# Performance work log

Hardware: AMD Instinct MI355X
Metric: run time of the kernel (lower is better)

Reference implementation:

```python
import jax, jax.numpy as jnp
import numpy as np

B, T, E = 2, 2048, 1024
NEXP, TOPK, INTER = 8, 2, 1408


def setup_inputs() -> dict:
    key = jax.random.key(0)
    ks = jax.random.split(key, 5)
    s = 0.02
    return {
        "x": jax.random.normal(ks[0], (B, T, E), dtype=jnp.float32),
        "gate_w": jax.random.normal(ks[1], (NEXP, E), dtype=jnp.float32) * s,
        "wg": jax.random.normal(ks[2], (NEXP, INTER, E), dtype=jnp.float32) * s,
        "wu": jax.random.normal(ks[3], (NEXP, INTER, E), dtype=jnp.float32) * s,
        "wd": jax.random.normal(ks[4], (NEXP, E, INTER), dtype=jnp.float32) * s,
    }


def reference(x, gate_w, wg, wu, wd):
    # Router: scores [B,T,NEXP], topk softmax over selected experts only
    scores = jnp.einsum("btd,ed->bte", x, gate_w)
    topk_scores, topk_idx = jax.lax.top_k(scores, TOPK)  # [B,T,K]
    topk_probs = jax.nn.softmax(topk_scores, axis=-1)
    # Scatter back to dense gating probs [B,T,NEXP] (topk indices are unique)
    onehot = jax.nn.one_hot(topk_idx, NEXP, dtype=x.dtype)  # [B,T,K,NEXP]
    gating = jnp.sum(onehot * topk_probs[..., None], axis=-2)  # [B,T,NEXP]
    # Dense compute-all-experts (faithful to the original module)
    g = jnp.einsum("btd,eid->btei", x, wg)  # [B,T,NEXP,INTER]
    u = jnp.einsum("btd,eid->btei", x, wu)
    h = jax.nn.silu(g) * u
    expert_out = jnp.einsum("btei,edi->bted", h, wd)  # [B,T,NEXP,E]
    y = jnp.sum(gating[..., None] * expert_out, axis=-2)  # [B,T,E]
    return y
```

## Files before the change

kernel.cpp:

```cpp
#include <hip/hip_runtime.h>
#include <hip/hip_bf16.h>
#include <stdint.h>

typedef __hip_bfloat16 bf16;
typedef __attribute__((ext_vector_type(8))) short short8;
typedef __attribute__((ext_vector_type(4))) float f32x4;

#define NTOK  4096
#define EDIM  1024
#define NEXPT 8
#define INTERD 1408
#define MAXP  4096
#define WELEM (NEXPT * INTERD * EDIM)

#define GL16(g, l) __builtin_amdgcn_global_load_lds( \
    (const __attribute__((address_space(1))) unsigned int*)(g), \
    (__attribute__((address_space(3))) unsigned int*)(l), 16, 0, 0)

#define WAIT_VM(n)   asm volatile("s_waitcnt vmcnt(" #n ")" ::: "memory")
#define BAR()        __builtin_amdgcn_s_barrier()
#define PRIO(n)      __builtin_amdgcn_s_setprio(n)

__global__ __launch_bounds__(256) void prep_kernel(const float* __restrict__ wg, bf16* __restrict__ wgb,
                                                   const float* __restrict__ wu, bf16* __restrict__ wub,
                                                   const float* __restrict__ wd, bf16* __restrict__ wdb,
                                                   const float* __restrict__ x,
                                                   const float* __restrict__ gw,
                                                   bf16* __restrict__ xb,
                                                   int* __restrict__ sel,
                                                   float* __restrict__ tprob) {
    int b = blockIdx.x;
    if (b < 3072) {
        const float* src; bf16* dst;
        if (b < 1024)      { src = wg; dst = wgb; }
        else if (b < 2048) { src = wu; dst = wub; b -= 1024; }
        else               { src = wd; dst = wdb; b -= 2048; }
        int i = (b * 256 + threadIdx.x) * 4;
        int stride = 1024 * 256 * 4;
        for (; i < WELEM; i += stride) {
            float4 v = *(const float4*)(src + i);
            ushort4 o; bf16 t;
            t = __float2bfloat16(v.x); o.x = *(unsigned short*)&t;
            t = __float2bfloat16(v.y); o.y = *(unsigned short*)&t;
            t = __float2bfloat16(v.z); o.z = *(unsigned short*)&t;
            t = __float2bfloat16(v.w); o.w = *(unsigned short*)&t;
            *(ushort4*)(dst + i) = o;
        }
        return;
    }
    int t = (b - 3072) * 4 + (threadIdx.x >> 6);
    int lane = threadIdx.x & 63;
    const float* xr = x + (size_t)t * EDIM;
    float xv[16];
#pragma unroll
    for (int j = 0; j < 4; j++) {
        float4 v = *(const float4*)(xr + lane * 16 + j * 4);
        xv[4 * j] = v.x; xv[4 * j + 1] = v.y; xv[4 * j + 2] = v.z; xv[4 * j + 3] = v.w;
    }
    bf16* xbr = xb + (size_t)t * EDIM;
#pragma unroll
    for (int j = 0; j < 4; j++) {
        ushort4 o; bf16 c;
        c = __float2bfloat16(xv[4 * j]);     o.x = *(unsigned short*)&c;
        c = __float2bfloat16(xv[4 * j + 1]); o.y = *(unsigned short*)&c;
        c = __float2bfloat16(xv[4 * j + 2]); o.z = *(unsigned short*)&c;
        c = __float2bfloat16(xv[4 * j + 3]); o.w = *(unsigned short*)&c;
        *(ushort4*)(xbr + lane * 16 + j * 4) = o;
    }
    double acc[NEXPT];
#pragma unroll
    for (int e = 0; e < NEXPT; e++) acc[e] = 0.0;
#pragma unroll
    for (int e = 0; e < NEXPT; e++) {
        const float* gr = gw + e * EDIM + lane * 16;
#pragma unroll
        for (int j = 0; j < 16; j++) acc[e] += (double)xv[j] * (double)gr[j];
    }
#pragma unroll
    for (int off = 32; off >= 1; off >>= 1) {
#pragma unroll
        for (int e = 0; e < NEXPT; e++) acc[e] += __shfl_xor(acc[e], off, 64);
    }
    if (lane == 0) {
        int e0 = 0; double s0 = acc[0];
        for (int e = 1; e < NEXPT; e++) if (acc[e] > s0) { s0 = acc[e]; e0 = e; }
        int e1 = -1; double s1 = -1e300;
        for (int e = 0; e < NEXPT; e++) if (e != e0 && acc[e] > s1) { s1 = acc[e]; e1 = e; }
        float z = __expf((float)(s1 - s0));
        float p0 = 1.f / (1.f + z);
        sel[t] = e0 | (e1 << 8);
        tprob[2 * t] = p0;
        tprob[2 * t + 1] = 1.f - p0;
    }
}

__global__ __launch_bounds__(512) void bucket_kernel(const int* __restrict__ sel,
                                                     const float* __restrict__ tprob,
                                                     int* __restrict__ counts,
                                                     int* __restrict__ offsets,
                                                     int* __restrict__ ptok,
                                                     float* __restrict__ pprob,
                                                     int* __restrict__ inv,
                                                     int* __restrict__ wq1,
                                                     int* __restrict__ wq2) {
    __shared__ int scnt[NEXPT];
    int w = threadIdx.x >> 6;
    int lane = threadIdx.x & 63;
    unsigned long long ltmask = (lane == 63) ? ~0ull >> 1 : (1ull << lane) - 1;
    int base = 0;
    for (int t0 = 0; t0 < NTOK; t0 += 64) {
        int t = t0 + lane;
        int s = sel[t];
        int e0 = s & 0xff, e1 = (s >> 8) & 0xff;
        unsigned long long m0 = __ballot(e0 == w);
        if (e0 == w) {
            int pos = base + __popcll(m0 & ltmask);
            ptok[w * MAXP + pos] = t;
            pprob[w * MAXP + pos] = tprob[2 * t];
            inv[2 * t] = (w << 16) | pos;
        }
        base += __popcll(m0);
        unsigned long long m1 = __ballot(e1 == w);
        if (e1 == w) {
            int pos = base + __popcll(m1 & ltmask);
            ptok[w * MAXP + pos] = t;
            pprob[w * MAXP + pos] = tprob[2 * t + 1];
            inv[2 * t + 1] = (w << 16) | pos;
        }
        base += __popcll(m1);
    }
    if (lane == 0) scnt[w] = base;
    __syncthreads();
    if (threadIdx.x < NEXPT) {
        int off = 0;
        for (int e = 0; e < (int)threadIdx.x; e++) off += scnt[e];
        counts[threadIdx.x] = scnt[threadIdx.x];
        offsets[threadIdx.x] = off;
        wq1[threadIdx.x * 32] = 0;
        wq2[threadIdx.x * 32] = 0;
    }
}

__global__ __launch_bounds__(512, 4) void gemm1_kernel(const bf16* __restrict__ xb,
                                                       const bf16* __restrict__ wgb,
                                                       const bf16* __restrict__ wub,
                                                       bf16* __restrict__ hout,
                                                       const int* __restrict__ counts,
                                                       const int* __restrict__ offsets,
                                                       const int* __restrict__ ptok,
                                                       const float* __restrict__ pprob,
                                                       int* __restrict__ wq1) {
    int eown = blockIdx.x & 7;

    __shared__ __align__(16) bf16 smem[3 * 12288];
    __shared__ int s_wi;

    int tid  = threadIdx.x;
    int lane = tid & 63;
    int wid  = tid >> 6;
    int wm   = wid >> 2;
    int wn   = wid & 3;

    int srow = tid >> 2;
    int qs   = (((tid & 3) ^ ((srow >> 1) & 3)) * 8);
    int l15  = lane & 15;
    int l4   = lane >> 4;

    int offA[4], offG[2];
#pragma unroll
    for (int m = 0; m < 4; m++) {
        int r = wm * 64 + m * 16 + l15;
        offA[m] = r * 32 + ((l4 ^ ((r >> 1) & 3)) * 8);
    }
#pragma unroll
    for (int n = 0; n < 2; n++) {
        int r = wn * 32 + n * 16 + l15;
        offG[n] = r * 32 + ((l4 ^ ((r >> 1) & 3)) * 8);
    }

    for (int ei = 0; ei < NEXPT; ++ei) {
        int e = (eown + ei) & 7;
        int cnt = counts[e];
        int mtiles = (cnt + 127) >> 7;
        int tiles = mtiles * (INTERD / 128);
        int hbase = offsets[e];

        for (;;) {
            if (tid == 0) s_wi = atomicAdd(&wq1[e * 32], 1);
            __syncthreads();
            int wi = s_wi;
            __syncthreads();
            if (wi >= tiles) break;
            int mt = wi % mtiles;
            int nt = wi / mtiles;
            int m0 = mt * 128;
            int n0 = nt * 128;

            WAIT_VM(0);
            const bf16* gA = xb + (size_t)ptok[e * MAXP + min(m0 + srow, cnt - 1)] * EDIM + qs;
            const bf16* gG = wgb + ((size_t)e * INTERD + n0 + srow) * EDIM + qs;
            const bf16* gU = wub + ((size_t)e * INTERD + n0 + srow) * EDIM + qs;

            f32x4 accg[4][2], accu[4][2];
#pragma unroll
            for (int m = 0; m < 4; m++)
#pragma unroll
                for (int n = 0; n < 2; n++) {
                    accg[m][n] = (f32x4){0.f, 0.f, 0.f, 0.f};
                    accu[m][n] = (f32x4){0.f, 0.f, 0.f, 0.f};
                }

#define SB1(t) (smem + ((t) % 3) * 12288)
#define G1_STAGE(t) do { bf16* sb_ = SB1(t); int ko_ = (t) * 32; \
            GL16(gA + ko_, sb_ + wid * 512); \
            GL16(gG + ko_, sb_ + 4096 + wid * 512); \
            GL16(gU + ko_, sb_ + 8192 + wid * 512); } while (0)

            G1_STAGE(0); G1_STAGE(1);

            for (int t = 0; t < 32; ++t) {
                if (t < 30)       { G1_STAGE(t + 2); WAIT_VM(6); }
                else if (t == 30) { WAIT_VM(3); }
                else              { WAIT_VM(0); }
                BAR();
                const bf16* sb = SB1(t);
                short8 a_[4], gf[2], uf[2];
#pragma unroll
                for (int m = 0; m < 4; m++) a_[m] = *(const short8*)&sb[offA[m]];
#pragma unroll
                for (int n = 0; n < 2; n++) {
                    gf[n] = *(const short8*)&sb[4096 + offG[n]];
                    uf[n] = *(const short8*)&sb[8192 + offG[n]];
                }
                PRIO(1);
#pragma unroll
                for (int m = 0; m < 4; m++)
#pragma unroll
                    for (int n = 0; n < 2; n++) {
                        accg[m][n] = __builtin_amdgcn_mfma_f32_16x16x32_bf16(a_[m], gf[n], accg[m][n], 0, 0, 0);
                        accu[m][n] = __builtin_amdgcn_mfma_f32_16x16x32_bf16(a_[m], uf[n], accu[m][n], 0, 0, 0);
                    }
                PRIO(0);
                BAR();
            }
#undef SB1
#undef G1_STAGE

#pragma unroll
            for (int m = 0; m < 4; m++)
#pragma unroll
                for (int n = 0; n < 2; n++)
#pragma unroll
                    for (int r = 0; r < 4; r++) {
                        int pos = m0 + wm * 64 + m * 16 + l4 * 4 + r;
                        if (pos < cnt) {
                            int col = n0 + wn * 32 + n * 16 + l15;
                            float p = pprob[e * MAXP + pos];
                            float gv = accg[m][n][r];
                            float uv = accu[m][n][r];
                            float hv = (gv / (1.f + __expf(-gv))) * uv * p;
                            hout[(size_t)(hbase + pos) * INTERD + col] = __float2bfloat16(hv);
                        }
                    }
        }
    }
}

__global__ __launch_bounds__(512, 4) void gemm2_kernel(const bf16* __restrict__ h,
                                                       const bf16* __restrict__ wdb,
                                                       bf16* __restrict__ out2,
                                                       const int* __restrict__ counts,
                                                       const int* __restrict__ offsets,
                                                       int* __restrict__ wq2) {
    int eown = blockIdx.x & 7;

    __shared__ __align__(16) bf16 smem[3 * 8192];
    __shared__ int s_wi;

    int tid  = threadIdx.x;
    int lane = tid & 63;
    int wid  = tid >> 6;
    int wm   = wid >> 2;
    int wn   = wid & 3;

    int srow = tid >> 2;
    int qs   = (((tid & 3) ^ ((srow >> 1) & 3)) * 8);
    int l15  = lane & 15;
    int l4   = lane >> 4;

    int offA[4], offB[2];
#pragma unroll
    for (int m = 0; m < 4; m++) {
        int r = wm * 64 + m * 16 + l15;
        offA[m] = r * 32 + ((l4 ^ ((r >> 1) & 3)) * 8);
    }
#pragma unroll
    for (int n = 0; n < 2; n++) {
        int r = wn * 32 + n * 16 + l15;
        offB[n] = 4096 + r * 32 + ((l4 ^ ((r >> 1) & 3)) * 8);
    }

    for (int ei = 0; ei < NEXPT; ++ei) {
        int e = (eown + ei) & 7;
        int cnt = counts[e];
        int mtiles = (cnt + 127) >> 7;
        int tiles = mtiles * (EDIM / 128);
        int hbase = offsets[e];

        for (;;) {
            if (tid == 0) s_wi = atomicAdd(&wq2[e * 32], 1);
            __syncthreads();
            int wi = s_wi;
            __syncthreads();
            if (wi >= tiles) break;
            int mt = wi % mtiles;
            int nt = wi / mtiles;
            int m0 = mt * 128;
            int n0 = nt * 128;

            WAIT_VM(0);
            const bf16* gA = h + (size_t)(hbase + min(m0 + srow, cnt - 1)) * INTERD + qs;
            const bf16* gB = wdb + ((size_t)e * EDIM + n0 + srow) * INTERD + qs;

            f32x4 acc[4][2];
#pragma unroll
            for (int m = 0; m < 4; m++)
#pragma unroll
                for (int n = 0; n < 2; n++) acc[m][n] = (f32x4){0.f, 0.f, 0.f, 0.f};

#define SB2(t) (smem + ((t) % 3) * 8192)
#define G2_STAGE(t) do { bf16* sb_ = SB2(t); int ko_ = (t) * 32; \
            GL16(gA + ko_, sb_ + wid * 512); \
            GL16(gB + ko_, sb_ + 4096 + wid * 512); } while (0)

            G2_STAGE(0); G2_STAGE(1);

            for (int t = 0; t < 44; ++t) {
                if (t < 42)       { G2_STAGE(t + 2); WAIT_VM(4); }
                else if (t == 42) { WAIT_VM(2); }
                else              { WAIT_VM(0); }
                BAR();
                const bf16* sb = SB2(t);
                short8 a_[4], b_[2];
#pragma unroll
                for (int m = 0; m < 4; m++) a_[m] = *(const short8*)&sb[offA[m]];
#pragma unroll
                for (int n = 0; n < 2; n++) b_[n] = *(const short8*)&sb[offB[n]];
                PRIO(1);
#pragma unroll
                for (int m = 0; m < 4; m++)
#pragma unroll
                    for (int n = 0; n < 2; n++)
                        acc[m][n] = __builtin_amdgcn_mfma_f32_16x16x32_bf16(a_[m], b_[n], acc[m][n], 0, 0, 0);
                PRIO(0);
                BAR();
            }
#undef SB2
#undef G2_STAGE

#pragma unroll
            for (int m = 0; m < 4; m++)
#pragma unroll
                for (int n = 0; n < 2; n++)
#pragma unroll
                    for (int r = 0; r < 4; r++) {
                        int pos = m0 + wm * 64 + m * 16 + l4 * 4 + r;
                        if (pos < cnt) {
                            int col = n0 + wn * 32 + n * 16 + l15;
                            out2[(size_t)(hbase + pos) * EDIM + col] = __float2bfloat16(acc[m][n][r]);
                        }
                    }
        }
    }
}

__global__ __launch_bounds__(256) void combine_kernel(const bf16* __restrict__ out2,
                                                      const int* __restrict__ inv,
                                                      const int* __restrict__ offsets,
                                                      float* __restrict__ y) {
    int idx = blockIdx.x * 256 + threadIdx.x;
    int t = idx >> 7;
    int c = (idx & 127) * 8;
    int a = inv[2 * t], b = inv[2 * t + 1];
    const short8 va = *(const short8*)(out2 + (size_t)(offsets[a >> 16] + (a & 0xFFFF)) * EDIM + c);
    const short8 vb = *(const short8*)(out2 + (size_t)(offsets[b >> 16] + (b & 0xFFFF)) * EDIM + c);
    float o[8];
#pragma unroll
    for (int j = 0; j < 8; j++) {
        unsigned ua = ((unsigned)(unsigned short)va[j]) << 16;
        unsigned ub = ((unsigned)(unsigned short)vb[j]) << 16;
        o[j] = *(float*)&ua + *(float*)&ub;
    }
    float* yp = y + (size_t)t * EDIM + c;
    *(float4*)yp       = (float4){o[0], o[1], o[2], o[3]};
    *(float4*)(yp + 4) = (float4){o[4], o[5], o[6], o[7]};
}

extern "C" void kernel_launch(void* const* d_in, const int* in_sizes, int n_in,
                              void* d_out, int out_size, void* d_ws, size_t ws_size,
                              hipStream_t stream) {
    const float* x      = (const float*)d_in[0];
    const float* gate_w = (const float*)d_in[1];
    const float* wg     = (const float*)d_in[2];
    const float* wu     = (const float*)d_in[3];
    const float* wd     = (const float*)d_in[4];
    float* y = (float*)d_out;

    char* ws = (char*)d_ws;
    constexpr size_t SZ_XB = (size_t)NTOK * EDIM * 2;
    constexpr size_t SZ_W  = (size_t)WELEM * 2;
    constexpr size_t SZ_H  = (size_t)NTOK * 2 * INTERD * 2;
    bf16* xb  = (bf16*)ws;
    bf16* wgb = (bf16*)(ws + SZ_XB);
    bf16* wub = (bf16*)(ws + SZ_XB + SZ_W);
    bf16* wdb = (bf16*)(ws + SZ_XB + 2 * SZ_W);
    bf16* h   = (bf16*)(ws + SZ_XB + 3 * SZ_W);
    char* meta = ws + SZ_XB + 3 * SZ_W + SZ_H;
    int*   counts  = (int*)meta;
    int*   offsets = (int*)(meta + 256);
    int*   ptok    = (int*)(meta + 512);
    float* pprob   = (float*)(meta + 512 + (size_t)NEXPT * MAXP * 4);
    int*   inv     = (int*)(meta + 512 + (size_t)NEXPT * MAXP * 8);
    char*  meta2   = meta + 512 + (size_t)NEXPT * MAXP * 8 + (size_t)NTOK * 2 * 4;
    int*   wq1     = (int*)meta2;
    int*   wq2     = (int*)(meta2 + 1024);
    int*   sel     = (int*)(meta2 + 2048);
    float* tprob   = (float*)(meta2 + 2048 + (size_t)NTOK * 4);
    bf16* out2 = (bf16*)(ws + SZ_XB);

    prep_kernel<<<3072 + NTOK / 4, 256, 0, stream>>>(wg, wgb, wu, wub, wd, wdb,
                                                     x, gate_w, xb, sel, tprob);
    bucket_kernel<<<1, 512, 0, stream>>>(sel, tprob, counts, offsets, ptok, pprob, inv,
                                         wq1, wq2);

    gemm1_kernel<<<512, 512, 0, stream>>>(
        xb, wgb, wub, h, counts, offsets, ptok, pprob, wq1);
    gemm2_kernel<<<512, 512, 0, stream>>>(
        h, wdb, out2, counts, offsets, wq2);
    combine_kernel<<<NTOK * EDIM / 8 / 256, 256, 0, stream>>>(out2, inv, offsets, y);
}
```

Measured before the change: 230.1 us.

## Fuse combine into gemm2 via atomic scatter-add and enlarge per-wave tile

Removes the separate combine kernel and the bf16 out2 intermediate. gemm2 now scatter-adds fp32 results directly into y using ptok and atomicAdd, and y is zeroed with a memset beforehand. gemm2 is also changed to 256 threads with each wave computing a 64x64 sub-tile, doubling MFMA work per LDS load. This trades the intermediate write/read and one launch for 8M float atomics, which may contend, and makes the summation order nondeterministic.

```diff
diff --git a/kernel.cpp b/kernel.cpp
--- a/kernel.cpp
+++ b/kernel.cpp
@@ -100,7 +100,6 @@
                                                      int* __restrict__ offsets,
                                                      int* __restrict__ ptok,
                                                      float* __restrict__ pprob,
-                                                     int* __restrict__ inv,
                                                      int* __restrict__ wq1,
                                                      int* __restrict__ wq2) {
     __shared__ int scnt[NEXPT];
@@ -117,7 +116,6 @@
             int pos = base + __popcll(m0 & ltmask);
             ptok[w * MAXP + pos] = t;
             pprob[w * MAXP + pos] = tprob[2 * t];
-            inv[2 * t] = (w << 16) | pos;
         }
         base += __popcll(m0);
         unsigned long long m1 = __ballot(e1 == w);
@@ -125,7 +123,6 @@
             int pos = base + __popcll(m1 & ltmask);
             ptok[w * MAXP + pos] = t;
             pprob[w * MAXP + pos] = tprob[2 * t + 1];
-            inv[2 * t + 1] = (w << 16) | pos;
         }
         base += __popcll(m1);
     }
@@ -266,11 +263,12 @@
     }
 }
 
-__global__ __launch_bounds__(512, 4) void gemm2_kernel(const bf16* __restrict__ h,
+__global__ __launch_bounds__(256, 2) void gemm2_kernel(const bf16* __restrict__ h,
                                                        const bf16* __restrict__ wdb,
-                                                       bf16* __restrict__ out2,
+                                                       float* __restrict__ y,
                                                        const int* __restrict__ counts,
                                                        const int* __restrict__ offsets,
+                                                       const int* __restrict__ ptok,
                                                        int* __restrict__ wq2) {
     int eown = blockIdx.x & 7;
 
@@ -280,23 +278,23 @@
     int tid  = threadIdx.x;
     int lane = tid & 63;
     int wid  = tid >> 6;
-    int wm   = wid >> 2;
-    int wn   = wid & 3;
+    int wm   = wid >> 1;
+    int wn   = wid & 1;
 
     int srow = tid >> 2;
     int qs   = (((tid & 3) ^ ((srow >> 1) & 3)) * 8);
     int l15  = lane & 15;
     int l4   = lane >> 4;
 
-    int offA[4], offB[2];
+    int offA[4], offB[4];
 #pragma unroll
     for (int m = 0; m < 4; m++) {
         int r = wm * 64 + m * 16 + l15;
         offA[m] = r * 32 + ((l4 ^ ((r >> 1) & 3)) * 8);
     }
 #pragma unroll
-    for (int n = 0; n < 2; n++) {
-        int r = wn * 32 + n * 16 + l15;
+    for (int n = 0; n < 4; n++) {
+        int r = wn * 64 + n * 16 + l15;
         offB[n] = 4096 + r * 32 + ((l4 ^ ((r >> 1) & 3)) * 8);
     }
 
@@ -319,38 +317,42 @@
             int n0 = nt * 128;
 
             WAIT_VM(0);
-            const bf16* gA = h + (size_t)(hbase + min(m0 + srow, cnt - 1)) * INTERD + qs;
-            const bf16* gB = wdb + ((size_t)e * EDIM + n0 + srow) * INTERD + qs;
-
-            f32x4 acc[4][2];
+            const bf16* gA0 = h + (size_t)(hbase + min(m0 + srow,      cnt - 1)) * INTERD + qs;
+            const bf16* gA1 = h + (size_t)(hbase + min(m0 + 64 + srow, cnt - 1)) * INTERD + qs;
+            const bf16* gB0 = wdb + ((size_t)e * EDIM + n0 + srow) * INTERD + qs;
+            const bf16* gB1 = wdb + ((size_t)e * EDIM + n0 + 64 + srow) * INTERD + qs;
+
+            f32x4 acc[4][4];
 #pragma unroll
             for (int m = 0; m < 4; m++)
 #pragma unroll
-                for (int n = 0; n < 2; n++) acc[m][n] = (f32x4){0.f, 0.f, 0.f, 0.f};
+                for (int n = 0; n < 4; n++) acc[m][n] = (f32x4){0.f, 0.f, 0.f, 0.f};
 
 #define SB2(t) (smem + ((t) % 3) * 8192)
 #define G2_STAGE(t) do { bf16* sb_ = SB2(t); int ko_ = (t) * 32; \
-            GL16(gA + ko_, sb_ + wid * 512); \
-            GL16(gB + ko_, sb_ + 4096 + wid * 512); } while (0)
+            GL16(gA0 + ko_, sb_ + wid * 512); \
+            GL16(gA1 + ko_, sb_ + 2048 + wid * 512); \
+            GL16(gB0 + ko_, sb_ + 4096 + wid * 512); \
+            GL16(gB1 + ko_, sb_ + 6144 + wid * 512); } while (0)
 
             G2_STAGE(0); G2_STAGE(1);
 
             for (int t = 0; t < 44; ++t) {
-                if (t < 42)       { G2_STAGE(t + 2); WAIT_VM(4); }
-                else if (t == 42) { WAIT_VM(2); }
+                if (t < 42)       { G2_STAGE(t + 2); WAIT_VM(8); }
+                else if (t == 42) { WAIT_VM(4); }
                 else              { WAIT_VM(0); }
                 BAR();
                 const bf16* sb = SB2(t);
-                short8 a_[4], b_[2];
+                short8 a_[4], b_[4];
 #pragma unroll
                 for (int m = 0; m < 4; m++) a_[m] = *(const short8*)&sb[offA[m]];
 #pragma unroll
-                for (int n = 0; n < 2; n++) b_[n] = *(const short8*)&sb[offB[n]];
+                for (int n = 0; n < 4; n++) b_[n] = *(const short8*)&sb[offB[n]];
                 PRIO(1);
 #pragma unroll
                 for (int m = 0; m < 4; m++)
 #pragma unroll
-                    for (int n = 0; n < 2; n++)
+                    for (int n = 0; n < 4; n++)
                         acc[m][n] = __builtin_amdgcn_mfma_f32_16x16x32_bf16(a_[m], b_[n], acc[m][n], 0, 0, 0);
                 PRIO(0);
                 BAR();
@@ -359,41 +361,23 @@
 #undef G2_STAGE
 
 #pragma unroll
-            for (int m = 0; m < 4; m++)
-#pragma unroll
-                for (int n = 0; n < 2; n++)
-#pragma unroll
-                    for (int r = 0; r < 4; r++) {
-                        int pos = m0 + wm * 64 + m * 16 + l4 * 4 + r;
-                        if (pos < cnt) {
-                            int col = n0 + wn * 32 + n * 16 + l15;
-                            out2[(size_t)(hbase + pos) * EDIM + col] = __float2bfloat16(acc[m][n][r]);
-                        }
-                    }
+            for (int m = 0; m < 4; m++) {
+                int pos = m0 + wm * 64 + m * 16 + l4 * 4;
+                int tok[4];
+#pragma unroll
+                for (int r = 0; r < 4; r++)
+                    tok[r] = (pos + r < cnt) ? ptok[e * MAXP + pos + r] : -1;
+#pragma unroll
+                for (int n = 0; n < 4; n++) {
+                    int col = n0 + wn * 64 + n * 16 + l15;
+#pragma unroll
+                    for (int r = 0; r < 4; r++)
+                        if (tok[r] >= 0)
+                            atomicAdd(&y[(size_t)tok[r] * EDIM + col], acc[m][n][r]);
+                }
+            }
         }
     }
-}
-
-__global__ __launch_bounds__(256) void combine_kernel(const bf16* __restrict__ out2,
-                                                      const int* __restrict__ inv,
-                                                      const int* __restrict__ offsets,
-                                                      float* __restrict__ y) {
-    int idx = blockIdx.x * 256 + threadIdx.x;
-    int t = idx >> 7;
-    int c = (idx & 127) * 8;
-    int a = inv[2 * t], b = inv[2 * t + 1];
-    const short8 va = *(const short8*)(out2 + (size_t)(offsets[a >> 16] + (a & 0xFFFF)) * EDIM + c);
-    const short8 vb = *(const short8*)(out2 + (size_t)(offsets[b >> 16] + (b & 0xFFFF)) * EDIM + c);
-    float o[8];
-#pragma unroll
-    for (int j = 0; j < 8; j++) {
-        unsigned ua = ((unsigned)(unsigned short)va[j]) << 16;
-        unsigned ub = ((unsigned)(unsigned short)vb[j]) << 16;
-        o[j] = *(float*)&ua + *(float*)&ub;
-    }
-    float* yp = y + (size_t)t * EDIM + c;
-    *(float4*)yp       = (float4){o[0], o[1], o[2], o[3]};
-    *(float4*)(yp + 4) = (float4){o[4], o[5], o[6], o[7]};
 }
 
 extern "C" void kernel_launch(void* const* d_in, const int* in_sizes, int n_in,
@@ -420,22 +404,21 @@
     int*   offsets = (int*)(meta + 256);
     int*   ptok    = (int*)(meta + 512);
     float* pprob   = (float*)(meta + 512 + (size_t)NEXPT * MAXP * 4);
-    int*   inv     = (int*)(meta + 512 + (size_t)NEXPT * MAXP * 8);
-    char*  meta2   = meta + 512 + (size_t)NEXPT * MAXP * 8 + (size_t)NTOK * 2 * 4;
+    char*  meta2   = meta + 512 + (size_t)NEXPT * MAXP * 8;
     int*   wq1     = (int*)meta2;
     int*   wq2     = (int*)(meta2 + 1024);
     int*   sel     = (int*)(meta2 + 2048);
     float* tprob   = (float*)(meta2 + 2048 + (size_t)NTOK * 4);
-    bf16* out2 = (bf16*)(ws + SZ_XB);
+
+    hipMemsetAsync(d_out, 0, (size_t)out_size * 4, stream);
 
     prep_kernel<<<3072 + NTOK / 4, 256, 0, stream>>>(wg, wgb, wu, wub, wd, wdb,
                                                      x, gate_w, xb, sel, tprob);
-    bucket_kernel<<<1, 512, 0, stream>>>(sel, tprob, counts, offsets, ptok, pprob, inv,
+    bucket_kernel<<<1, 512, 0, stream>>>(sel, tprob, counts, offsets, ptok, pprob,
                                          wq1, wq2);
 
     gemm1_kernel<<<512, 512, 0, stream>>>(
         xb, wgb, wub, h, counts, offsets, ptok, pprob, wq1);
-    gemm2_kernel<<<512, 512, 0, stream>>>(
-        h, wdb, out2, counts, offsets, wq2);
-    combine_kernel<<<NTOK * EDIM / 8 / 256, 256, 0, stream>>>(out2, inv, offsets, y);
+    gemm2_kernel<<<512, 256, 0, stream>>>(
+        h, wdb, y, counts, offsets, ptok, wq2);
 }
```

Result: slower. 249.8 us (+8.6%).

## Widen gemm2 tiles to 128x256 and replace atomic work queue with static grid

Applied to the files above, without the earlier changes.

The down-projection GEMM now uses 128x256 output tiles, so each wave computes a 64x64 sub-tile and each A tile loaded into shared memory feeds twice as many MFMAs. The atomic-counter work queue is replaced by a fixed grid of 256 blocks indexed by expert, M-slot and N-tile, and each block strides over M in steps of 1024. This removes the per-tile atomic and the barriers around it and increases reuse of the A tile. In exchange it uses more accumulator registers and LDS, and load balance across experts becomes static, so a skewed routing distribution can leave some blocks with more work than others.

```diff
diff --git a/kernel.cpp b/kernel.cpp
--- a/kernel.cpp
+++ b/kernel.cpp
@@ -270,12 +270,16 @@
                                                        const bf16* __restrict__ wdb,
                                                        bf16* __restrict__ out2,
                                                        const int* __restrict__ counts,
-                                                       const int* __restrict__ offsets,
-                                                       int* __restrict__ wq2) {
-    int eown = blockIdx.x & 7;
-
-    __shared__ __align__(16) bf16 smem[3 * 8192];
-    __shared__ int s_wi;
+                                                       const int* __restrict__ offsets) {
+    int bx = blockIdx.x;
+    int e  = bx & 7;
+    int mt = (bx >> 3) & 7;
+    int nt = bx >> 6;
+    int cnt = counts[e];
+    int n0 = nt * 256;
+    int hbase = offsets[e];
+
+    __shared__ __align__(16) bf16 smem[3 * 12288];
 
     int tid  = threadIdx.x;
     int lane = tid & 63;
@@ -288,89 +292,74 @@
     int l15  = lane & 15;
     int l4   = lane >> 4;
 
-    int offA[4], offB[2];
+    int offA[4], offB[4];
 #pragma unroll
     for (int m = 0; m < 4; m++) {
         int r = wm * 64 + m * 16 + l15;
         offA[m] = r * 32 + ((l4 ^ ((r >> 1) & 3)) * 8);
     }
 #pragma unroll
-    for (int n = 0; n < 2; n++) {
-        int r = wn * 32 + n * 16 + l15;
+    for (int n = 0; n < 4; n++) {
+        int r = wn * 64 + n * 16 + l15;
         offB[n] = 4096 + r * 32 + ((l4 ^ ((r >> 1) & 3)) * 8);
     }
 
-    for (int ei = 0; ei < NEXPT; ++ei) {
-        int e = (eown + ei) & 7;
-        int cnt = counts[e];
-        int mtiles = (cnt + 127) >> 7;
-        int tiles = mtiles * (EDIM / 128);
-        int hbase = offsets[e];
-
-        for (;;) {
-            if (tid == 0) s_wi = atomicAdd(&wq2[e * 32], 1);
-            __syncthreads();
-            int wi = s_wi;
-            __syncthreads();
-            if (wi >= tiles) break;
-            int mt = wi % mtiles;
-            int nt = wi / mtiles;
-            int m0 = mt * 128;
-            int n0 = nt * 128;
-
-            WAIT_VM(0);
-            const bf16* gA = h + (size_t)(hbase + min(m0 + srow, cnt - 1)) * INTERD + qs;
-            const bf16* gB = wdb + ((size_t)e * EDIM + n0 + srow) * INTERD + qs;
-
-            f32x4 acc[4][2];
+    const bf16* gB0 = wdb + ((size_t)e * EDIM + n0 + srow) * INTERD + qs;
+    const bf16* gB1 = wdb + ((size_t)e * EDIM + n0 + 128 + srow) * INTERD + qs;
+
+    for (int m0 = mt * 128; m0 < cnt; m0 += 1024) {
+        WAIT_VM(0);
+        const bf16* gA = h + (size_t)(hbase + min(m0 + srow, cnt - 1)) * INTERD + qs;
+
+        f32x4 acc[4][4];
+#pragma unroll
+        for (int m = 0; m < 4; m++)
+#pragma unroll
+            for (int n = 0; n < 4; n++) acc[m][n] = (f32x4){0.f, 0.f, 0.f, 0.f};
+
+#define SB2(t) (smem + ((t) % 3) * 12288)
+#define G2_STAGE(t) do { bf16* sb_ = SB2(t); int ko_ = (t) * 32; \
+        GL16(gA + ko_,  sb_ + wid * 512); \
+        GL16(gB0 + ko_, sb_ + 4096 + wid * 512); \
+        GL16(gB1 + ko_, sb_ + 8192 + wid * 512); } while (0)
+
+        G2_STAGE(0); G2_STAGE(1);
+
+        for (int t = 0; t < 44; ++t) {
+            if (t < 42)       { G2_STAGE(t + 2); WAIT_VM(6); }
+            else if (t == 42) { WAIT_VM(3); }
+            else              { WAIT_VM(0); }
+            BAR();
+            const bf16* sb = SB2(t);
+            short8 a_[4], b_[4];
+#pragma unroll
+            for (int m = 0; m < 4; m++) a_[m] = *(const short8*)&sb[offA[m]];
+#pragma unroll
+            for (int n = 0; n < 4; n++) b_[n] = *(const short8*)&sb[offB[n]];
+            PRIO(1);
 #pragma unroll
             for (int m = 0; m < 4; m++)
 #pragma unroll
-                for (int n = 0; n < 2; n++) acc[m][n] = (f32x4){0.f, 0.f, 0.f, 0.f};
-
-#define SB2(t) (smem + ((t) % 3) * 8192)
-#define G2_STAGE(t) do { bf16* sb_ = SB2(t); int ko_ = (t) * 32; \
-            GL16(gA + ko_, sb_ + wid * 512); \
-            GL16(gB + ko_, sb_ + 4096 + wid * 512); } while (0)
-
-            G2_STAGE(0); G2_STAGE(1);
-
-            for (int t = 0; t < 44; ++t) {
-                if (t < 42)       { G2_STAGE(t + 2); WAIT_VM(4); }
-                else if (t == 42) { WAIT_VM(2); }
-                else              { WAIT_VM(0); }
-                BAR();
-                const bf16* sb = SB2(t);
-                short8 a_[4], b_[2];
-#pragma unroll
-                for (int m = 0; m < 4; m++) a_[m] = *(const short8*)&sb[offA[m]];
-#pragma unroll
-                for (int n = 0; n < 2; n++) b_[n] = *(const short8*)&sb[offB[n]];
-                PRIO(1);
-#pragma unroll
-                for (int m = 0; m < 4; m++)
-#pragma unroll
-                    for (int n = 0; n < 2; n++)
-                        acc[m][n] = __builtin_amdgcn_mfma_f32_16x16x32_bf16(a_[m], b_[n], acc[m][n], 0, 0, 0);
-                PRIO(0);
-                BAR();
-            }
+                for (int n = 0; n < 4; n++)
+                    acc[m][n] = __builtin_amdgcn_mfma_f32_16x16x32_bf16(a_[m], b_[n], acc[m][n], 0, 0, 0);
+            PRIO(0);
+            BAR();
+        }
 #undef SB2
 #undef G2_STAGE
 
 #pragma unroll
-            for (int m = 0; m < 4; m++)
-#pragma unroll
-                for (int n = 0; n < 2; n++)
-#pragma unroll
-                    for (int r = 0; r < 4; r++) {
-                        int pos = m0 + wm * 64 + m * 16 + l4 * 4 + r;
-                        if (pos < cnt) {
-                            int col = n0 + wn * 32 + n * 16 + l15;
-                            out2[(size_t)(hbase + pos) * EDIM + col] = __float2bfloat16(acc[m][n][r]);
-                        }
+        for (int m = 0; m < 4; m++)
+#pragma unroll
+            for (int n = 0; n < 4; n++)
+#pragma unroll
+                for (int r = 0; r < 4; r++) {
+                    int pos = m0 + wm * 64 + m * 16 + l4 * 4 + r;
+                    if (pos < cnt) {
+                        int col = n0 + wn * 64 + n * 16 + l15;
+                        out2[(size_t)(hbase + pos) * EDIM + col] = __float2bfloat16(acc[m][n][r]);
                     }
-        }
+                }
     }
 }
 
@@ -435,7 +424,7 @@
 
     gemm1_kernel<<<512, 512, 0, stream>>>(
         xb, wgb, wub, h, counts, offsets, ptok, pprob, wq1);
-    gemm2_kernel<<<512, 512, 0, stream>>>(
-        h, wdb, out2, counts, offsets, wq2);
+    gemm2_kernel<<<NEXPT * 8 * (EDIM / 256), 512, 0, stream>>>(
+        h, wdb, out2, counts, offsets);
     combine_kernel<<<NTOK * EDIM / 8 / 256, 256, 0, stream>>>(out2, inv, offsets, y);
 }
```

After: 219.4 us, median of 3. -4.6%, faster.

## Split K across wave groups in down-projection GEMM with LDS reduction

Applied to the files above, without the earlier changes.

Reorganizes the gemm2 kernel so the 8 waves form two K-groups of four, each wave computing a 64x64 sub-tile over half of a 64-wide K step. It replaces the triple-buffered 32-wide K pipeline with double-buffered 64-wide stages and a wider XOR swizzle, then reduces the two K-group partial accumulators through LDS before writing out. The goal is more MFMA work per LDS fragment load and fewer barriers per tile. The cost is more accumulator registers, an extra LDS reduction with two syncs per tile, and shallower prefetch.

```diff
diff --git a/kernel.cpp b/kernel.cpp
--- a/kernel.cpp
+++ b/kernel.cpp
@@ -274,30 +274,32 @@
                                                        int* __restrict__ wq2) {
     int eown = blockIdx.x & 7;
 
-    __shared__ __align__(16) bf16 smem[3 * 8192];
+    __shared__ __align__(16) bf16 smem[2 * 16384];
     __shared__ int s_wi;
 
     int tid  = threadIdx.x;
     int lane = tid & 63;
     int wid  = tid >> 6;
-    int wm   = wid >> 2;
-    int wn   = wid & 3;
-
-    int srow = tid >> 2;
-    int qs   = (((tid & 3) ^ ((srow >> 1) & 3)) * 8);
+    int pair = wid & 3;
+    int wm   = pair >> 1;
+    int wn   = pair & 1;
+    int wk   = wid >> 2;
+
+    int srow = tid >> 3;
+    int qs   = (((tid & 7) ^ (srow & 7)) * 8);
     int l15  = lane & 15;
     int l4   = lane >> 4;
 
-    int offA[4], offB[2];
+    int offA[4], offB[4];
 #pragma unroll
     for (int m = 0; m < 4; m++) {
         int r = wm * 64 + m * 16 + l15;
-        offA[m] = r * 32 + ((l4 ^ ((r >> 1) & 3)) * 8);
-    }
-#pragma unroll
-    for (int n = 0; n < 2; n++) {
-        int r = wn * 32 + n * 16 + l15;
-        offB[n] = 4096 + r * 32 + ((l4 ^ ((r >> 1) & 3)) * 8);
+        offA[m] = r * 64 + (((wk * 4 + l4) ^ (r & 7)) * 8);
+    }
+#pragma unroll
+    for (int n = 0; n < 4; n++) {
+        int r = wn * 64 + n * 16 + l15;
+        offB[n] = 8192 + r * 64 + (((wk * 4 + l4) ^ (r & 7)) * 8);
     }
 
     for (int ei = 0; ei < NEXPT; ++ei) {
@@ -319,38 +321,41 @@
             int n0 = nt * 128;
 
             WAIT_VM(0);
-            const bf16* gA = h + (size_t)(hbase + min(m0 + srow, cnt - 1)) * INTERD + qs;
-            const bf16* gB = wdb + ((size_t)e * EDIM + n0 + srow) * INTERD + qs;
-
-            f32x4 acc[4][2];
+            const bf16* gA0 = h + (size_t)(hbase + min(m0 + srow,      cnt - 1)) * INTERD + qs;
+            const bf16* gA1 = h + (size_t)(hbase + min(m0 + 64 + srow, cnt - 1)) * INTERD + qs;
+            const bf16* gB0 = wdb + ((size_t)e * EDIM + n0 + srow) * INTERD + qs;
+            const bf16* gB1 = wdb + ((size_t)e * EDIM + n0 + 64 + srow) * INTERD + qs;
+
+            f32x4 acc[4][4];
 #pragma unroll
             for (int m = 0; m < 4; m++)
 #pragma unroll
-                for (int n = 0; n < 2; n++) acc[m][n] = (f32x4){0.f, 0.f, 0.f, 0.f};
-
-#define SB2(t) (smem + ((t) % 3) * 8192)
-#define G2_STAGE(t) do { bf16* sb_ = SB2(t); int ko_ = (t) * 32; \
-            GL16(gA + ko_, sb_ + wid * 512); \
-            GL16(gB + ko_, sb_ + 4096 + wid * 512); } while (0)
-
-            G2_STAGE(0); G2_STAGE(1);
-
-            for (int t = 0; t < 44; ++t) {
-                if (t < 42)       { G2_STAGE(t + 2); WAIT_VM(4); }
-                else if (t == 42) { WAIT_VM(2); }
-                else              { WAIT_VM(0); }
+                for (int n = 0; n < 4; n++) acc[m][n] = (f32x4){0.f, 0.f, 0.f, 0.f};
+
+#define SB2(t) (smem + ((t) & 1) * 16384)
+#define G2_STAGE(t) do { bf16* sb_ = SB2(t); int ko_ = (t) * 64; \
+            GL16(gA0 + ko_, sb_ + wid * 512); \
+            GL16(gA1 + ko_, sb_ + 4096 + wid * 512); \
+            GL16(gB0 + ko_, sb_ + 8192 + wid * 512); \
+            GL16(gB1 + ko_, sb_ + 12288 + wid * 512); } while (0)
+
+            G2_STAGE(0);
+
+            for (int t = 0; t < 22; ++t) {
+                if (t < 21) { G2_STAGE(t + 1); WAIT_VM(4); }
+                else        { WAIT_VM(0); }
                 BAR();
                 const bf16* sb = SB2(t);
-                short8 a_[4], b_[2];
+                short8 a_[4], b_[4];
 #pragma unroll
                 for (int m = 0; m < 4; m++) a_[m] = *(const short8*)&sb[offA[m]];
 #pragma unroll
-                for (int n = 0; n < 2; n++) b_[n] = *(const short8*)&sb[offB[n]];
+                for (int n = 0; n < 4; n++) b_[n] = *(const short8*)&sb[offB[n]];
                 PRIO(1);
 #pragma unroll
                 for (int m = 0; m < 4; m++)
 #pragma unroll
-                    for (int n = 0; n < 2; n++)
+                    for (int n = 0; n < 4; n++)
                         acc[m][n] = __builtin_amdgcn_mfma_f32_16x16x32_bf16(a_[m], b_[n], acc[m][n], 0, 0, 0);
                 PRIO(0);
                 BAR();
@@ -358,18 +363,43 @@
 #undef SB2
 #undef G2_STAGE
 
-#pragma unroll
-            for (int m = 0; m < 4; m++)
-#pragma unroll
-                for (int n = 0; n < 2; n++)
-#pragma unroll
-                    for (int r = 0; r < 4; r++) {
-                        int pos = m0 + wm * 64 + m * 16 + l4 * 4 + r;
-                        if (pos < cnt) {
-                            int col = n0 + wn * 32 + n * 16 + l15;
-                            out2[(size_t)(hbase + pos) * EDIM + col] = __float2bfloat16(acc[m][n][r]);
+            float* fbuf = (float*)smem;
+            if (wk == 1) {
+#pragma unroll
+                for (int m = 0; m < 4; m++)
+#pragma unroll
+                    for (int n = 0; n < 4; n++) {
+                        int i = (m * 4 + n) * 4;
+                        int a = pair * 4096 + lane * 64 + (i ^ ((lane & 15) << 2));
+                        *(f32x4*)&fbuf[a] = acc[m][n];
+                    }
+            }
+            __syncthreads();
+            if (wk == 0) {
+#pragma unroll
+                for (int m = 0; m < 4; m++)
+#pragma unroll
+                    for (int n = 0; n < 4; n++) {
+                        int i = (m * 4 + n) * 4;
+                        int a = pair * 4096 + lane * 64 + (i ^ ((lane & 15) << 2));
+                        f32x4 v = *(const f32x4*)&fbuf[a];
+                        acc[m][n][0] += v[0]; acc[m][n][1] += v[1];
+                        acc[m][n][2] += v[2]; acc[m][n][3] += v[3];
+                    }
+#pragma unroll
+                for (int m = 0; m < 4; m++)
+#pragma unroll
+                    for (int n = 0; n < 4; n++)
+#pragma unroll
+                        for (int r = 0; r < 4; r++) {
+                            int pos = m0 + wm * 64 + m * 16 + l4 * 4 + r;
+                            if (pos < cnt) {
+                                int col = n0 + wn * 64 + n * 16 + l15;
+                                out2[(size_t)(hbase + pos) * EDIM + col] = __float2bfloat16(acc[m][n][r]);
+                            }
                         }
-                    }
+            }
+            __syncthreads();
         }
     }
 }
```

Result: slower. 258.5 us (+12.4%).
